# Kernel optimization log

Measured on AMD Instinct MI355X. Metric: run time of the kernel, lower is better.

## Reference

```python
import jax, jax.numpy as jnp
import numpy as np

EMBED_DIM = 1024
HEAD_SIZE = 64
B, T = 4, 4096


def setup_inputs() -> dict:
    key = jax.random.key(0)
    kx, kq, kk, kv = jax.random.split(key, 4)
    x = jax.random.normal(kx, (B, T, EMBED_DIM), dtype=jnp.float32)
    sw = 1.0 / np.sqrt(EMBED_DIM)  # kaiming-ish init scale for linear weights
    Wq = jax.random.normal(kq, (EMBED_DIM, HEAD_SIZE), dtype=jnp.float32) * sw
    Wk = jax.random.normal(kk, (EMBED_DIM, HEAD_SIZE), dtype=jnp.float32) * sw
    Wv = jax.random.normal(kv, (EMBED_DIM, HEAD_SIZE), dtype=jnp.float32) * sw
    return {"x": x, "Wq": Wq, "Wk": Wk, "Wv": Wv}


def reference(x, Wq, Wk, Wv):
    Bn, Tn, C = x.shape
    q = jnp.einsum('btc,ch->bth', x, Wq)
    k = jnp.einsum('btc,ch->bth', x, Wk)
    v = jnp.einsum('btc,ch->bth', x, Wv)
    # NOTE: original scales by sqrt(C) = sqrt(embed_dim), not sqrt(head_size)
    scale = 1.0 / jnp.sqrt(jnp.asarray(C, dtype=x.dtype))
    wei = jnp.einsum('bth,bsh->bts', q, k) * scale  # [B, T, T]
    causal = jnp.tril(jnp.ones((Tn, Tn), dtype=bool))
    wei = jnp.where(causal, wei, -jnp.inf)
    wei = jax.nn.softmax(wei, axis=-1)
    # dropout p=0.0 (eval mode): identity
    return jnp.einsum('bts,bsh->bth', wei, v)
```

## Files before the change

### kernel.cpp

```cpp
#include <hip/hip_runtime.h>
#include <cstdint>


typedef __bf16 bf16;
typedef __bf16 bf16x8 __attribute__((ext_vector_type(8)));
typedef float  f32x4  __attribute__((ext_vector_type(4)));

#define MFMA16(a, b, c) __builtin_amdgcn_mfma_f32_16x16x32_bf16((a), (b), (c), 0, 0, 0)

#if __has_builtin(__builtin_amdgcn_exp2f)
#define EXP2(x) __builtin_amdgcn_exp2f(x)
#else
#define EXP2(x) exp2f(x)
#endif

#define B_SZ 4
#define T_SZ 4096
#define C_SZ 1024
#define H_SZ 64
#define M_SZ (B_SZ * T_SZ)
#define QSCALE (1.4426950408889634f / 32.0f)
#define P_STR 4160

__device__ __forceinline__ void dma16(const void* g, void* l) {
    __builtin_amdgcn_global_load_lds(
        (const __attribute__((address_space(1))) uint32_t*)(uintptr_t)g,
        (__attribute__((address_space(3))) uint32_t*)(uint32_t)(uintptr_t)l,
        16, 0, 0);
}

__global__ __launch_bounds__(256) void wt_prep(
    const float* __restrict__ Wq, const float* __restrict__ Wk,
    const float* __restrict__ Wv, bf16* __restrict__ wt2)
{
    const int n4 = blockIdx.x, t = threadIdx.x;
    const int nbase = n4 * 4;
    const float* W = (nbase < 64) ? Wq : (nbase < 128 ? Wk : Wv);
    const float sc = (nbase < 64) ? QSCALE : 1.0f;
    const int ncol = nbase & 63;
    #pragma unroll
    for (int i = 0; i < 4; ++i) {
        const int k = i * 256 + t;
        const float4 v = *(const float4*)(W + (size_t)k * H_SZ + ncol);
        const float vals[4] = {v.x, v.y, v.z, v.w};
        const size_t base = (size_t)(k >> 6) * 12288 + (size_t)((k >> 5) & 1) * 6144
                          + (size_t)((k >> 3) & 3) * 1536 + (k & 7);
        #pragma unroll
        for (int m = 0; m < 4; ++m)
            wt2[base + (size_t)(nbase + m) * 8] = (bf16)(vals[m] * sc);
    }
}

__global__ __launch_bounds__(256) void qkv_proj(
    const float* __restrict__ x, const bf16* __restrict__ wt2,
    bf16* __restrict__ qw, bf16* __restrict__ kw2, bf16* __restrict__ vtw2)
{
    const int m0 = blockIdx.x * 32;
    const int tid = threadIdx.x;
    const int wave = tid >> 6, lane = tid & 63;
    const int quad = lane >> 4, l15 = lane & 15;
    const int phase = blockIdx.x & 15;

    __shared__ __align__(16) float xs[2 * 4 * 32 * 8];
    __shared__ __align__(16) bf16  ws[2 * 4 * 192 * 8];

    f32x4 acc[2][3] = {};

    const char* xg = (const char*)x
        + (size_t)(m0 + ((tid >> 1) & 31)) * 4096
        + (size_t)((tid >> 6) & 3) * 32 + (size_t)(tid & 1) * 16;
    char* xl = (char*)xs + (size_t)tid * 16;
    const char* wg = (const char*)wt2 + (size_t)tid * 16;
    char* wl = (char*)ws + (size_t)tid * 16;

    for (int s = 0; s < 16; ++s) {
        const size_t se = (size_t)((s + phase) & 15);
        __syncthreads();
        dma16(xg + se * 256, xl);
        dma16(xg + se * 256 + 128, xl + 4096);
        #pragma unroll
        for (int i = 0; i < 6; ++i)
            dma16(wg + se * 24576 + (size_t)i * 4096, wl + (size_t)i * 4096);
        __syncthreads();

        #pragma unroll
        for (int ss = 0; ss < 2; ++ss) {
            bf16x8 a[2];
            #pragma unroll
            for (int mg = 0; mg < 2; ++mg) {
                const float* ap = xs + ss * 1024 + quad * 256 + (mg * 16 + l15) * 8;
                const f32x4 lo = *(const f32x4*)ap;
                const f32x4 hi = *(const f32x4*)(ap + 4);
                a[mg][0] = (bf16)lo[0]; a[mg][1] = (bf16)lo[1];
                a[mg][2] = (bf16)lo[2]; a[mg][3] = (bf16)lo[3];
                a[mg][4] = (bf16)hi[0]; a[mg][5] = (bf16)hi[1];
                a[mg][6] = (bf16)hi[2]; a[mg][7] = (bf16)hi[3];
            }
            #pragma unroll
            for (int i = 0; i < 3; ++i) {
                const int nt = wave * 3 + i;
                const bf16x8 wf = *(const bf16x8*)(ws + ss * 6144 + quad * 1536
                                                   + (nt * 16 + l15) * 8);
                #pragma unroll
                for (int mg = 0; mg < 2; ++mg)
                    acc[mg][i] = MFMA16(a[mg], wf, acc[mg][i]);
            }
        }
    }

    #pragma unroll
    for (int mg = 0; mg < 2; ++mg)
        #pragma unroll
        for (int i = 0; i < 3; ++i) {
            const int n = (wave * 3 + i) * 16 + l15;
            const int which = n >> 6, col = n & 63;
            #pragma unroll
            for (int r = 0; r < 4; ++r) {
                const int t = m0 + mg * 16 + quad * 4 + r;
                const bf16 v = (bf16)acc[mg][i][r];
                if (which == 0) {
                    qw[(size_t)t * H_SZ + col] = v;
                } else if (which == 1) {
                    kw2[(size_t)(t >> 6) * 4096
                        + (size_t)(((col >> 5) << 2) + ((col >> 3) & 3)) * 512
                        + (size_t)(t & 63) * 8 + (col & 7)] = v;
                } else {
                    vtw2[(size_t)(t >> 6) * 4096
                         + (size_t)((((t >> 5) & 1) << 2) + ((t >> 3) & 3)) * 512
                         + (size_t)col * 8 + (t & 7)] = v;
                }
            }
        }
}

__global__ __launch_bounds__(256) void flash_attn(
    const bf16* __restrict__ qw, const bf16* __restrict__ kw2,
    const bf16* __restrict__ vtw2, float* __restrict__ pbuf)
{
    const int bx = blockIdx.x;
    const int item = (bx & 1) ? (1023 - (bx >> 1)) : (bx >> 1);
    const int qt = 63 - (item >> 4);
    const int b  = (item >> 2) & 3;
    const int h  = item & 3;
    const int i0 = qt * 64;
    const int nkv = qt + 1;

    const int tid = threadIdx.x;
    const int mg = tid >> 6, lane = tid & 63;
    const int quad = lane >> 4, l15 = lane & 15;

    __shared__ __align__(16) bf16 kvs[8192];
    __shared__ __align__(16) bf16 pls[4][16 * 72];

    bf16x8 aq0, aq1;
    {
        const bf16* qp = qw + ((size_t)b * T_SZ + i0 + mg * 16 + l15) * H_SZ + quad * 8;
        aq0 = *(const bf16x8*)qp;
        aq1 = *(const bf16x8*)(qp + 32);
    }
    const bf16 onev = (bf16)1.0f;
    const bf16x8 vone = {onev, onev, onev, onev, onev, onev, onev, onev};

    const char* kgb = (const char*)kw2 + (size_t)b * 524288;
    const char* vgb = (const char*)vtw2 + (size_t)b * 524288;
    const bf16* kb = kvs;
    const bf16* vb = kvs + 4096;
    bf16* pl = pls[mg];

    f32x4 o[4] = {};
    f32x4 osum = {};

    for (int jt = h; jt < nkv; jt += 4) {
        __syncthreads();
        {
            const char* ks = kgb + (size_t)jt * 8192;
            const char* vs = vgb + (size_t)jt * 8192;
            char* dst = (char*)kvs + (size_t)tid * 16;
            dma16(ks + (size_t)tid * 16, dst);
            dma16(ks + 4096 + (size_t)tid * 16, dst + 4096);
            dma16(vs + (size_t)tid * 16, dst + 8192);
            dma16(vs + 4096 + (size_t)tid * 16, dst + 12288);
        }
        __syncthreads();

        f32x4 s4[4] = {};
        #pragma unroll
        for (int ct = 0; ct < 4; ++ct) {
            const bf16x8 k0 = *(const bf16x8*)(kb + (0 * 4 + quad) * 512 + (ct * 16 + l15) * 8);
            const bf16x8 k1 = *(const bf16x8*)(kb + (1 * 4 + quad) * 512 + (ct * 16 + l15) * 8);
            s4[ct] = MFMA16(aq0, k0, s4[ct]);
            s4[ct] = MFMA16(aq1, k1, s4[ct]);
        }
        if (jt == qt) {
            #pragma unroll
            for (int ct = 0; ct < 4; ++ct) {
                const int col = ct * 16 + l15;
                const int row = mg * 16 + quad * 4;
                #pragma unroll
                for (int rr = 0; rr < 4; ++rr)
                    if (col > row + rr) s4[ct][rr] = -3.0e38f;
            }
        }
        #pragma unroll
        for (int ct = 0; ct < 4; ++ct)
            #pragma unroll
            for (int rr = 0; rr < 4; ++rr)
                pl[(quad * 4 + rr) * 72 + ct * 16 + l15] = (bf16)EXP2(s4[ct][rr]);
        const bf16x8 pa0 = *(const bf16x8*)&pl[l15 * 72 + quad * 8];
        const bf16x8 pa1 = *(const bf16x8*)&pl[l15 * 72 + 32 + quad * 8];

        #pragma unroll
        for (int ht = 0; ht < 4; ++ht) {
            const bf16x8 v0 = *(const bf16x8*)(vb + (0 * 4 + quad) * 512 + (ht * 16 + l15) * 8);
            const bf16x8 v1 = *(const bf16x8*)(vb + (1 * 4 + quad) * 512 + (ht * 16 + l15) * 8);
            o[ht] = MFMA16(pa0, v0, o[ht]);
            o[ht] = MFMA16(pa1, v1, o[ht]);
        }
        osum = MFMA16(pa0, vone, osum);
        osum = MFMA16(pa1, vone, osum);
    }

    float* pb = pbuf + (size_t)(((b * 64 + qt) * 4) + h) * P_STR;
    #pragma unroll
    for (int ht = 0; ht < 4; ++ht)
        #pragma unroll
        for (int rr = 0; rr < 4; ++rr)
            pb[(mg * 16 + quad * 4 + rr) * 64 + ht * 16 + l15] = o[ht][rr];
    if (l15 == 0) {
        #pragma unroll
        for (int rr = 0; rr < 4; ++rr)
            pb[4096 + mg * 16 + quad * 4 + rr] = osum[rr];
    }
}

__global__ __launch_bounds__(256) void combine(
    const float* __restrict__ pbuf, float* __restrict__ out)
{
    const int bq = blockIdx.x, tid = threadIdx.x;
    const int row = tid >> 2, c0 = (tid & 3) * 16;
    const float* p = pbuf + (size_t)bq * 4 * P_STR;

    f32x4 a0 = {}, a1 = {}, a2 = {}, a3 = {};
    float l = 0.f;
    #pragma unroll
    for (int h = 0; h < 4; ++h) {
        const float* ph = p + (size_t)h * P_STR + row * 64 + c0;
        a0 += *(const f32x4*)(ph);
        a1 += *(const f32x4*)(ph + 4);
        a2 += *(const f32x4*)(ph + 8);
        a3 += *(const f32x4*)(ph + 12);
        l  += p[(size_t)h * P_STR + 4096 + row];
    }
    const float inv = 1.0f / l;
    float* op = out + ((size_t)bq * 64 + row) * 64 + c0;
    *(f32x4*)(op)      = a0 * inv;
    *(f32x4*)(op + 4)  = a1 * inv;
    *(f32x4*)(op + 8)  = a2 * inv;
    *(f32x4*)(op + 12) = a3 * inv;
}

extern "C" void kernel_launch(void* const* d_in, const int* in_sizes, int n_in,
                              void* d_out, int out_size, void* d_ws, size_t ws_size,
                              hipStream_t stream) {
    const float* x  = (const float*)d_in[0];
    const float* Wq = (const float*)d_in[1];
    const float* Wk = (const float*)d_in[2];
    const float* Wv = (const float*)d_in[3];

    bf16* qw   = (bf16*)d_ws;
    bf16* kw2  = qw + (size_t)M_SZ * H_SZ;
    bf16* vtw2 = kw2 + (size_t)M_SZ * H_SZ;
    bf16* wt2  = vtw2 + (size_t)M_SZ * H_SZ;
    float* pbuf = (float*)(wt2 + 3 * 64 * 1024);
    float* out = (float*)d_out;

    wt_prep<<<48, 256, 0, stream>>>(Wq, Wk, Wv, wt2);
    qkv_proj<<<M_SZ / 32, 256, 0, stream>>>(x, wt2, qw, kw2, vtw2);
    flash_attn<<<1024, 256, 0, stream>>>(qw, kw2, vtw2, pbuf);
    combine<<<256, 256, 0, stream>>>(pbuf, out);
}
```

Baseline: 146.7 us.

## Double-buffer LDS staging in projection and attention, add MFMA priority hints

```diff
diff --git a/kernel.cpp b/kernel.cpp
--- a/kernel.cpp
+++ b/kernel.cpp
@@ -27,6 +27,12 @@
         (const __attribute__((address_space(1))) uint32_t*)(uintptr_t)g,
         (__attribute__((address_space(3))) uint32_t*)(uint32_t)(uintptr_t)l,
         16, 0, 0);
+}
+
+__device__ __forceinline__ void pipe_sync() {
+    asm volatile("s_waitcnt vmcnt(0)" ::: "memory");
+    __builtin_amdgcn_s_barrier();
+    __builtin_amdgcn_sched_barrier(0);
 }
 
 __global__ __launch_bounds__(256) void wt_prep(
@@ -61,34 +67,41 @@
     const int quad = lane >> 4, l15 = lane & 15;
     const int phase = blockIdx.x & 15;
 
-    __shared__ __align__(16) float xs[2 * 4 * 32 * 8];
-    __shared__ __align__(16) bf16  ws[2 * 4 * 192 * 8];
+    __shared__ __align__(16) float xs[2][2 * 4 * 32 * 8];
+    __shared__ __align__(16) bf16  ws[2][2 * 4 * 192 * 8];
 
     f32x4 acc[2][3] = {};
 
     const char* xg = (const char*)x
         + (size_t)(m0 + ((tid >> 1) & 31)) * 4096
         + (size_t)((tid >> 6) & 3) * 32 + (size_t)(tid & 1) * 16;
-    char* xl = (char*)xs + (size_t)tid * 16;
     const char* wg = (const char*)wt2 + (size_t)tid * 16;
-    char* wl = (char*)ws + (size_t)tid * 16;
-
-    for (int s = 0; s < 16; ++s) {
+
+    auto stage = [&](int s, int buf) {
         const size_t se = (size_t)((s + phase) & 15);
-        __syncthreads();
+        char* xl = (char*)(&xs[buf][0]) + (size_t)tid * 16;
+        char* wl = (char*)(&ws[buf][0]) + (size_t)tid * 16;
         dma16(xg + se * 256, xl);
         dma16(xg + se * 256 + 128, xl + 4096);
         #pragma unroll
         for (int i = 0; i < 6; ++i)
             dma16(wg + se * 24576 + (size_t)i * 4096, wl + (size_t)i * 4096);
-        __syncthreads();
+    };
+
+    stage(0, 0);
+    pipe_sync();
+
+    for (int s = 0; s < 16; ++s) {
+        if (s < 15) stage(s + 1, (s + 1) & 1);
+        const float* xb = &xs[s & 1][0];
+        const bf16*  wb = &ws[s & 1][0];
 
         #pragma unroll
         for (int ss = 0; ss < 2; ++ss) {
             bf16x8 a[2];
             #pragma unroll
             for (int mg = 0; mg < 2; ++mg) {
-                const float* ap = xs + ss * 1024 + quad * 256 + (mg * 16 + l15) * 8;
+                const float* ap = xb + ss * 1024 + quad * 256 + (mg * 16 + l15) * 8;
                 const f32x4 lo = *(const f32x4*)ap;
                 const f32x4 hi = *(const f32x4*)(ap + 4);
                 a[mg][0] = (bf16)lo[0]; a[mg][1] = (bf16)lo[1];
@@ -99,13 +112,15 @@
             #pragma unroll
             for (int i = 0; i < 3; ++i) {
                 const int nt = wave * 3 + i;
-                const bf16x8 wf = *(const bf16x8*)(ws + ss * 6144 + quad * 1536
+                const bf16x8 wf = *(const bf16x8*)(wb + ss * 6144 + quad * 1536
                                                    + (nt * 16 + l15) * 8);
                 #pragma unroll
                 for (int mg = 0; mg < 2; ++mg)
                     acc[mg][i] = MFMA16(a[mg], wf, acc[mg][i]);
             }
         }
+
+        pipe_sync();
     }
 
     #pragma unroll
@@ -149,7 +164,7 @@
     const int mg = tid >> 6, lane = tid & 63;
     const int quad = lane >> 4, l15 = lane & 15;
 
-    __shared__ __align__(16) bf16 kvs[8192];
+    __shared__ __align__(16) bf16 kvs[2][8192];
     __shared__ __align__(16) bf16 pls[4][16 * 72];
 
     bf16x8 aq0, aq1;
@@ -163,27 +178,34 @@
 
     const char* kgb = (const char*)kw2 + (size_t)b * 524288;
     const char* vgb = (const char*)vtw2 + (size_t)b * 524288;
-    const bf16* kb = kvs;
-    const bf16* vb = kvs + 4096;
     bf16* pl = pls[mg];
 
     f32x4 o[4] = {};
     f32x4 osum = {};
 
-    for (int jt = h; jt < nkv; jt += 4) {
-        __syncthreads();
-        {
-            const char* ks = kgb + (size_t)jt * 8192;
-            const char* vs = vgb + (size_t)jt * 8192;
-            char* dst = (char*)kvs + (size_t)tid * 16;
-            dma16(ks + (size_t)tid * 16, dst);
-            dma16(ks + 4096 + (size_t)tid * 16, dst + 4096);
-            dma16(vs + (size_t)tid * 16, dst + 8192);
-            dma16(vs + 4096 + (size_t)tid * 16, dst + 12288);
-        }
-        __syncthreads();
+    auto stage = [&](int jt, int buf) {
+        const char* ks = kgb + (size_t)jt * 8192;
+        const char* vs = vgb + (size_t)jt * 8192;
+        char* dst = (char*)(&kvs[buf][0]) + (size_t)tid * 16;
+        dma16(ks + (size_t)tid * 16, dst);
+        dma16(ks + 4096 + (size_t)tid * 16, dst + 4096);
+        dma16(vs + (size_t)tid * 16, dst + 8192);
+        dma16(vs + 4096 + (size_t)tid * 16, dst + 12288);
+    };
+
+    if (h < nkv) {
+        stage(h, 0);
+        pipe_sync();
+    }
+
+    int c = 0;
+    for (int jt = h; jt < nkv; jt += 4, c ^= 1) {
+        if (jt + 4 < nkv) stage(jt + 4, c ^ 1);
+        const bf16* kb = &kvs[c][0];
+        const bf16* vb = &kvs[c][0] + 4096;
 
         f32x4 s4[4] = {};
+        __builtin_amdgcn_s_setprio(1);
         #pragma unroll
         for (int ct = 0; ct < 4; ++ct) {
             const bf16x8 k0 = *(const bf16x8*)(kb + (0 * 4 + quad) * 512 + (ct * 16 + l15) * 8);
@@ -191,6 +213,7 @@
             s4[ct] = MFMA16(aq0, k0, s4[ct]);
             s4[ct] = MFMA16(aq1, k1, s4[ct]);
         }
+        __builtin_amdgcn_s_setprio(0);
         if (jt == qt) {
             #pragma unroll
             for (int ct = 0; ct < 4; ++ct) {
@@ -209,6 +232,7 @@
         const bf16x8 pa0 = *(const bf16x8*)&pl[l15 * 72 + quad * 8];
         const bf16x8 pa1 = *(const bf16x8*)&pl[l15 * 72 + 32 + quad * 8];
 
+        __builtin_amdgcn_s_setprio(1);
         #pragma unroll
         for (int ht = 0; ht < 4; ++ht) {
             const bf16x8 v0 = *(const bf16x8*)(vb + (0 * 4 + quad) * 512 + (ht * 16 + l15) * 8);
@@ -218,6 +242,9 @@
         }
         osum = MFMA16(pa0, vone, osum);
         osum = MFMA16(pa1, vone, osum);
+        __builtin_amdgcn_s_setprio(0);
+
+        pipe_sync();
     }
 
     float* pb = pbuf + (size_t)(((b * 64 + qt) * 4) + h) * P_STR;
@@ -236,27 +263,24 @@
 __global__ __launch_bounds__(256) void combine(
     const float* __restrict__ pbuf, float* __restrict__ out)
 {
-    const int bq = blockIdx.x, tid = threadIdx.x;
-    const int row = tid >> 2, c0 = (tid & 3) * 16;
+    const int bq = blockIdx.x >> 1, tid = threadIdx.x;
+    const int row = ((blockIdx.x & 1) << 5) + (tid >> 3);
+    const int c0 = (tid & 7) * 8;
     const float* p = pbuf + (size_t)bq * 4 * P_STR;
 
-    f32x4 a0 = {}, a1 = {}, a2 = {}, a3 = {};
+    f32x4 a0 = {}, a1 = {};
     float l = 0.f;
     #pragma unroll
     for (int h = 0; h < 4; ++h) {
         const float* ph = p + (size_t)h * P_STR + row * 64 + c0;
         a0 += *(const f32x4*)(ph);
         a1 += *(const f32x4*)(ph + 4);
-        a2 += *(const f32x4*)(ph + 8);
-        a3 += *(const f32x4*)(ph + 12);
         l  += p[(size_t)h * P_STR + 4096 + row];
     }
     const float inv = 1.0f / l;
     float* op = out + ((size_t)bq * 64 + row) * 64 + c0;
-    *(f32x4*)(op)      = a0 * inv;
-    *(f32x4*)(op + 4)  = a1 * inv;
-    *(f32x4*)(op + 8)  = a2 * inv;
-    *(f32x4*)(op + 12) = a3 * inv;
+    *(f32x4*)(op)     = a0 * inv;
+    *(f32x4*)(op + 4) = a1 * inv;
 }
 
 extern "C" void kernel_launch(void* const* d_in, const int* in_sizes, int n_in,
@@ -277,5 +301,5 @@
     wt_prep<<<48, 256, 0, stream>>>(Wq, Wk, Wv, wt2);
     qkv_proj<<<M_SZ / 32, 256, 0, stream>>>(x, wt2, qw, kw2, vtw2);
     flash_attn<<<1024, 256, 0, stream>>>(qw, kw2, vtw2, pbuf);
-    combine<<<256, 256, 0, stream>>>(pbuf, out);
-}
+    combine<<<512, 256, 0, stream>>>(pbuf, out);
+}
```

Result: slower. 152.2 us (+3.7%).

## Double-buffer KV tiles and process 128 query rows per attention block

Applied to the files above, without the earlier changes.

```diff
diff --git a/kernel.cpp b/kernel.cpp
--- a/kernel.cpp
+++ b/kernel.cpp
@@ -20,13 +20,19 @@
 #define H_SZ 64
 #define M_SZ (B_SZ * T_SZ)
 #define QSCALE (1.4426950408889634f / 32.0f)
-#define P_STR 4160
+#define P_STR 8320
 
 __device__ __forceinline__ void dma16(const void* g, void* l) {
     __builtin_amdgcn_global_load_lds(
         (const __attribute__((address_space(1))) uint32_t*)(uintptr_t)g,
         (__attribute__((address_space(3))) uint32_t*)(uint32_t)(uintptr_t)l,
         16, 0, 0);
+}
+
+__device__ __forceinline__ void pipe_sync() {
+    asm volatile("s_waitcnt vmcnt(0)" ::: "memory");
+    __builtin_amdgcn_s_barrier();
+    __builtin_amdgcn_sched_barrier(0);
 }
 
 __global__ __launch_bounds__(256) void wt_prep(
@@ -138,107 +144,148 @@
     const bf16* __restrict__ vtw2, float* __restrict__ pbuf)
 {
     const int bx = blockIdx.x;
-    const int item = (bx & 1) ? (1023 - (bx >> 1)) : (bx >> 1);
-    const int qt = 63 - (item >> 4);
-    const int b  = (item >> 2) & 3;
-    const int h  = item & 3;
-    const int i0 = qt * 64;
-    const int nkv = qt + 1;
+    const int item = (bx & 1) ? (511 - (bx >> 1)) : (bx >> 1);
+    const int qt2 = 31 - (item >> 4);
+    const int b   = (item >> 2) & 3;
+    const int h   = item & 3;
+    const int i0  = qt2 * 128;
+    const int nkv = qt2 * 2 + 2;
 
     const int tid = threadIdx.x;
-    const int mg = tid >> 6, lane = tid & 63;
+    const int wave = tid >> 6, lane = tid & 63;
     const int quad = lane >> 4, l15 = lane & 15;
 
-    __shared__ __align__(16) bf16 kvs[8192];
-    __shared__ __align__(16) bf16 pls[4][16 * 72];
-
-    bf16x8 aq0, aq1;
-    {
-        const bf16* qp = qw + ((size_t)b * T_SZ + i0 + mg * 16 + l15) * H_SZ + quad * 8;
-        aq0 = *(const bf16x8*)qp;
-        aq1 = *(const bf16x8*)(qp + 32);
+    __shared__ __align__(16) bf16 kvs[2][8192];
+    __shared__ __align__(16) bf16 pls[4][32 * 72];
+
+    bf16x8 aq[2][2];
+    #pragma unroll
+    for (int mg2 = 0; mg2 < 2; ++mg2) {
+        const bf16* qp = qw + ((size_t)b * T_SZ + i0 + wave * 32 + mg2 * 16 + l15) * H_SZ
+                       + quad * 8;
+        aq[mg2][0] = *(const bf16x8*)qp;
+        aq[mg2][1] = *(const bf16x8*)(qp + 32);
     }
     const bf16 onev = (bf16)1.0f;
     const bf16x8 vone = {onev, onev, onev, onev, onev, onev, onev, onev};
 
     const char* kgb = (const char*)kw2 + (size_t)b * 524288;
     const char* vgb = (const char*)vtw2 + (size_t)b * 524288;
-    const bf16* kb = kvs;
-    const bf16* vb = kvs + 4096;
-    bf16* pl = pls[mg];
-
-    f32x4 o[4] = {};
-    f32x4 osum = {};
-
-    for (int jt = h; jt < nkv; jt += 4) {
-        __syncthreads();
-        {
-            const char* ks = kgb + (size_t)jt * 8192;
-            const char* vs = vgb + (size_t)jt * 8192;
-            char* dst = (char*)kvs + (size_t)tid * 16;
-            dma16(ks + (size_t)tid * 16, dst);
-            dma16(ks + 4096 + (size_t)tid * 16, dst + 4096);
-            dma16(vs + (size_t)tid * 16, dst + 8192);
-            dma16(vs + 4096 + (size_t)tid * 16, dst + 12288);
-        }
-        __syncthreads();
-
-        f32x4 s4[4] = {};
+    bf16* pl = pls[wave];
+
+    f32x4 o[2][4] = {};
+    f32x4 osum[2] = {};
+
+    auto stage = [&](int jt, int buf) {
+        const char* ks = kgb + (size_t)jt * 8192;
+        const char* vs = vgb + (size_t)jt * 8192;
+        char* dst = (char*)(&kvs[buf][0]) + (size_t)tid * 16;
+        dma16(ks + (size_t)tid * 16, dst);
+        dma16(ks + 4096 + (size_t)tid * 16, dst + 4096);
+        dma16(vs + (size_t)tid * 16, dst + 8192);
+        dma16(vs + 4096 + (size_t)tid * 16, dst + 12288);
+    };
+
+    if (h < nkv) {
+        stage(h, 0);
+        pipe_sync();
+    }
+
+    int c = 0;
+    for (int jt = h; jt < nkv; jt += 4, c ^= 1) {
+        if (jt + 4 < nkv) stage(jt + 4, c ^ 1);
+        const bf16* kb = &kvs[c][0];
+        const bf16* vb = &kvs[c][0] + 4096;
+
+        f32x4 s4[2][4] = {};
+        __builtin_amdgcn_s_setprio(1);
         #pragma unroll
         for (int ct = 0; ct < 4; ++ct) {
             const bf16x8 k0 = *(const bf16x8*)(kb + (0 * 4 + quad) * 512 + (ct * 16 + l15) * 8);
             const bf16x8 k1 = *(const bf16x8*)(kb + (1 * 4 + quad) * 512 + (ct * 16 + l15) * 8);
-            s4[ct] = MFMA16(aq0, k0, s4[ct]);
-            s4[ct] = MFMA16(aq1, k1, s4[ct]);
-        }
-        if (jt == qt) {
-            #pragma unroll
-            for (int ct = 0; ct < 4; ++ct) {
-                const int col = ct * 16 + l15;
-                const int row = mg * 16 + quad * 4;
+            #pragma unroll
+            for (int mg2 = 0; mg2 < 2; ++mg2) {
+                s4[mg2][ct] = MFMA16(aq[mg2][0], k0, s4[mg2][ct]);
+                s4[mg2][ct] = MFMA16(aq[mg2][1], k1, s4[mg2][ct]);
+            }
+        }
+        __builtin_amdgcn_s_setprio(0);
+
+        if (jt >= 2 * qt2) {
+            #pragma unroll
+            for (int mg2 = 0; mg2 < 2; ++mg2) {
+                const int grow = i0 + wave * 32 + mg2 * 16 + quad * 4;
+                #pragma unroll
+                for (int ct = 0; ct < 4; ++ct) {
+                    const int gcol = jt * 64 + ct * 16 + l15;
+                    #pragma unroll
+                    for (int rr = 0; rr < 4; ++rr)
+                        if (gcol > grow + rr) s4[mg2][ct][rr] = -3.0e38f;
+                }
+            }
+        }
+
+        #pragma unroll
+        for (int mg2 = 0; mg2 < 2; ++mg2)
+            #pragma unroll
+            for (int ct = 0; ct < 4; ++ct)
                 #pragma unroll
                 for (int rr = 0; rr < 4; ++rr)
-                    if (col > row + rr) s4[ct][rr] = -3.0e38f;
-            }
-        }
-        #pragma unroll
-        for (int ct = 0; ct < 4; ++ct)
-            #pragma unroll
-            for (int rr = 0; rr < 4; ++rr)
-                pl[(quad * 4 + rr) * 72 + ct * 16 + l15] = (bf16)EXP2(s4[ct][rr]);
-        const bf16x8 pa0 = *(const bf16x8*)&pl[l15 * 72 + quad * 8];
-        const bf16x8 pa1 = *(const bf16x8*)&pl[l15 * 72 + 32 + quad * 8];
-
+                    pl[(mg2 * 16 + quad * 4 + rr) * 72 + ct * 16 + l15]
+                        = (bf16)EXP2(s4[mg2][ct][rr]);
+
+        bf16x8 pa[2][2];
+        #pragma unroll
+        for (int mg2 = 0; mg2 < 2; ++mg2) {
+            pa[mg2][0] = *(const bf16x8*)&pl[(mg2 * 16 + l15) * 72 + quad * 8];
+            pa[mg2][1] = *(const bf16x8*)&pl[(mg2 * 16 + l15) * 72 + 32 + quad * 8];
+        }
+
+        __builtin_amdgcn_s_setprio(1);
         #pragma unroll
         for (int ht = 0; ht < 4; ++ht) {
             const bf16x8 v0 = *(const bf16x8*)(vb + (0 * 4 + quad) * 512 + (ht * 16 + l15) * 8);
             const bf16x8 v1 = *(const bf16x8*)(vb + (1 * 4 + quad) * 512 + (ht * 16 + l15) * 8);
-            o[ht] = MFMA16(pa0, v0, o[ht]);
-            o[ht] = MFMA16(pa1, v1, o[ht]);
-        }
-        osum = MFMA16(pa0, vone, osum);
-        osum = MFMA16(pa1, vone, osum);
-    }
-
-    float* pb = pbuf + (size_t)(((b * 64 + qt) * 4) + h) * P_STR;
-    #pragma unroll
-    for (int ht = 0; ht < 4; ++ht)
-        #pragma unroll
-        for (int rr = 0; rr < 4; ++rr)
-            pb[(mg * 16 + quad * 4 + rr) * 64 + ht * 16 + l15] = o[ht][rr];
-    if (l15 == 0) {
-        #pragma unroll
-        for (int rr = 0; rr < 4; ++rr)
-            pb[4096 + mg * 16 + quad * 4 + rr] = osum[rr];
+            #pragma unroll
+            for (int mg2 = 0; mg2 < 2; ++mg2) {
+                o[mg2][ht] = MFMA16(pa[mg2][0], v0, o[mg2][ht]);
+                o[mg2][ht] = MFMA16(pa[mg2][1], v1, o[mg2][ht]);
+            }
+        }
+        #pragma unroll
+        for (int mg2 = 0; mg2 < 2; ++mg2) {
+            osum[mg2] = MFMA16(pa[mg2][0], vone, osum[mg2]);
+            osum[mg2] = MFMA16(pa[mg2][1], vone, osum[mg2]);
+        }
+        __builtin_amdgcn_s_setprio(0);
+
+        pipe_sync();
+    }
+
+    float* pb = pbuf + (size_t)(((b * 32 + qt2) * 4) + h) * P_STR;
+    #pragma unroll
+    for (int mg2 = 0; mg2 < 2; ++mg2) {
+        const int L0 = wave * 32 + mg2 * 16 + quad * 4;
+        #pragma unroll
+        for (int ht = 0; ht < 4; ++ht)
+            #pragma unroll
+            for (int rr = 0; rr < 4; ++rr)
+                pb[(L0 + rr) * 64 + ht * 16 + l15] = o[mg2][ht][rr];
+        if (l15 == 0) {
+            #pragma unroll
+            for (int rr = 0; rr < 4; ++rr)
+                pb[8192 + L0 + rr] = osum[mg2][rr];
+        }
     }
 }
 
 __global__ __launch_bounds__(256) void combine(
     const float* __restrict__ pbuf, float* __restrict__ out)
 {
-    const int bq = blockIdx.x, tid = threadIdx.x;
-    const int row = tid >> 2, c0 = (tid & 3) * 16;
-    const float* p = pbuf + (size_t)bq * 4 * P_STR;
+    const int bq2 = blockIdx.x >> 1, tid = threadIdx.x;
+    const int row = ((blockIdx.x & 1) << 6) + (tid >> 2);
+    const int c0 = (tid & 3) * 16;
+    const float* p = pbuf + (size_t)bq2 * 4 * P_STR;
 
     f32x4 a0 = {}, a1 = {}, a2 = {}, a3 = {};
     float l = 0.f;
@@ -249,10 +296,10 @@
         a1 += *(const f32x4*)(ph + 4);
         a2 += *(const f32x4*)(ph + 8);
         a3 += *(const f32x4*)(ph + 12);
-        l  += p[(size_t)h * P_STR + 4096 + row];
+        l  += p[(size_t)h * P_STR + 8192 + row];
     }
     const float inv = 1.0f / l;
-    float* op = out + ((size_t)bq * 64 + row) * 64 + c0;
+    float* op = out + ((size_t)bq2 * 128 + row) * 64 + c0;
     *(f32x4*)(op)      = a0 * inv;
     *(f32x4*)(op + 4)  = a1 * inv;
     *(f32x4*)(op + 8)  = a2 * inv;
@@ -276,6 +323,6 @@
 
     wt_prep<<<48, 256, 0, stream>>>(Wq, Wk, Wv, wt2);
     qkv_proj<<<M_SZ / 32, 256, 0, stream>>>(x, wt2, qw, kw2, vtw2);
-    flash_attn<<<1024, 256, 0, stream>>>(qw, kw2, vtw2, pbuf);
+    flash_attn<<<512, 256, 0, stream>>>(qw, kw2, vtw2, pbuf);
     combine<<<256, 256, 0, stream>>>(pbuf, out);
 }
```

New measurement: 148.7 us. No clear change (+1.3%).
